# Kernel optimization log

Hardware: AMD Instinct MI355X
Metric: run time of the kernel (lower is better)

Reference implementation:

```python
import jax, jax.numpy as jnp
import numpy as np

WIN = (4, 8, 8)          # window_size (wd, wh, ww)
NUM_HEADS = 8
NW = 64                  # number of distinct shift-mask windows


def _relative_position_index(win):
    wd, wh, ww = win
    coords = np.stack(np.meshgrid(np.arange(wd), np.arange(wh), np.arange(ww), indexing='ij'))
    flat = coords.reshape(3, -1)                       # (3, N)
    rel = flat[:, :, None] - flat[:, None, :]          # (3, N, N)
    rel = rel.transpose(1, 2, 0).astype(np.int64)      # (N, N, 3)
    rel[..., 0] += wd - 1
    rel[..., 1] += wh - 1
    rel[..., 2] += ww - 1
    rel[..., 0] *= (2 * wh - 1) * (2 * ww - 1)
    rel[..., 1] *= (2 * ww - 1)
    return rel.sum(-1)                                 # (N, N)


def setup_inputs() -> dict:
    key = jax.random.key(0)
    ks = jax.random.split(key, 8)
    B_, C = 192, 256
    N = WIN[0] * WIN[1] * WIN[2]                       # 256 tokens per window
    table = (2 * WIN[0] - 1) * (2 * WIN[1] - 1) * (2 * WIN[2] - 1)  # 1575
    s = 0.02
    return {
        'x': jax.random.normal(ks[0], (B_, N, C), jnp.float32),
        'mask': jax.random.normal(ks[1], (NW, N, N), jnp.float32),
        'qkv_w': jax.random.normal(ks[2], (3 * C, C), jnp.float32) * s,
        'qkv_b': jax.random.normal(ks[3], (3 * C,), jnp.float32) * s,
        'proj_w': jax.random.normal(ks[4], (C, C), jnp.float32) * s,
        'proj_b': jax.random.normal(ks[5], (C,), jnp.float32) * s,
        'rel_pos_table': jax.random.normal(ks[6], (table, NUM_HEADS), jnp.float32) * s,
        'rel_pos_index': jnp.asarray(_relative_position_index(WIN), jnp.int32),
    }


def reference(x, mask, qkv_w, qkv_b, proj_w, proj_b, rel_pos_table, rel_pos_index):
    B_, N, C = x.shape
    H = NUM_HEADS
    hd = C // H
    scale = hd ** -0.5
    # qkv projection -> (3, B_, H, N, hd)
    qkv = (x @ qkv_w.T + qkv_b).reshape(B_, N, 3, H, hd).transpose(2, 0, 3, 1, 4)
    q, k, v = qkv[0], qkv[1], qkv[2]
    attn = jnp.einsum('bhnd,bhmd->bhnm', q * scale, k)            # (B_, H, N, N)
    # gathered relative-position bias: (N, N, H) -> (H, N, N)
    bias = rel_pos_table[rel_pos_index.reshape(-1)].reshape(N, N, H).transpose(2, 0, 1)
    attn = attn + bias[None]
    nW = mask.shape[0]
    attn = attn.reshape(B_ // nW, nW, H, N, N) + mask[None, :, None]
    attn = jax.nn.softmax(attn.reshape(B_, H, N, N), axis=-1)
    out = jnp.einsum('bhnm,bhmd->bhnd', attn, v)                  # (B_, H, N, hd)
    out = out.transpose(0, 2, 1, 3).reshape(B_, N, C)
    return out @ proj_w.T + proj_b
```

## Files before the change

kernel.cpp:

```cpp
#include <hip/hip_runtime.h>

typedef unsigned short ushort_t;
typedef __bf16 bf16x8 __attribute__((ext_vector_type(8)));
typedef float floatx4 __attribute__((ext_vector_type(4)));
typedef float floatx16 __attribute__((ext_vector_type(16)));

#define B_WIN 192
#define NTOK 256
#define CDIM 256
#define NHEAD 8
#define HDIM 32
#define NWIN 64
#define MROWS (B_WIN * NTOK)
#define LOG2E 1.4426950408889634f

__device__ __forceinline__ float uasf(unsigned int u) {
  float f; __builtin_memcpy(&f, &u, 4); return f;
}
__device__ __forceinline__ ushort_t f2bf(float f) {
  unsigned int u; __builtin_memcpy(&u, &f, 4);
  u = (u + 0x7fffu + ((u >> 16) & 1u)) >> 16;
  return (ushort_t)u;
}
__device__ __forceinline__ bf16x8 ldg8(const ushort_t* p) {
  return *reinterpret_cast<const bf16x8*>(p);
}
__device__ __forceinline__ void async_copy16(const void* g, void* l) {
  __builtin_amdgcn_global_load_lds(
      (const __attribute__((address_space(1))) unsigned int*)g,
      (__attribute__((address_space(3))) unsigned int*)l, 16, 0, 0);
}
__device__ __forceinline__ float fexp2(float x) {
  return __builtin_amdgcn_exp2f(x);
}
__device__ __forceinline__ unsigned pkbf(float a, float b) {
  return (unsigned)f2bf(a) | ((unsigned)f2bf(b) << 16);
}
__device__ __forceinline__ void plswap(unsigned& a, unsigned& b) {
  auto r = __builtin_amdgcn_permlane32_swap(a, b, false, false);
  a = r[0]; b = r[1];
}

__global__ __launch_bounds__(256) void cvt_f32_bf16(const float* __restrict__ src,
                                                    ushort_t* __restrict__ dst, int n8) {
  int t = blockIdx.x * 256 + threadIdx.x;
  if (t >= n8) return;
  const float4* s = reinterpret_cast<const float4*>(src) + (size_t)t * 2;
  float4 v0 = s[0], v1 = s[1];
  union { ushort_t u[8]; uint4 v; } pk;
  pk.u[0] = f2bf(v0.x); pk.u[1] = f2bf(v0.y); pk.u[2] = f2bf(v0.z); pk.u[3] = f2bf(v0.w);
  pk.u[4] = f2bf(v1.x); pk.u[5] = f2bf(v1.y); pk.u[6] = f2bf(v1.z); pk.u[7] = f2bf(v1.w);
  reinterpret_cast<uint4*>(dst)[t] = pk.v;
}

__global__ __launch_bounds__(256) void cvt_tile_w(const float* __restrict__ src,
                                                  ushort_t* __restrict__ dst, int n) {
  int t = blockIdx.x * 256 + threadIdx.x;
  if (t >= n) return;
  int col = t >> 5;
  int kk = (t & 31) * 8;
  const float4* s = reinterpret_cast<const float4*>(src + (size_t)col * 256 + kk);
  float4 v0 = s[0], v1 = s[1];
  union { ushort_t u[8]; uint4 v; } pk;
  pk.u[0] = f2bf(v0.x); pk.u[1] = f2bf(v0.y); pk.u[2] = f2bf(v0.z); pk.u[3] = f2bf(v0.w);
  pk.u[4] = f2bf(v1.x); pk.u[5] = f2bf(v1.y); pk.u[6] = f2bf(v1.z); pk.u[7] = f2bf(v1.w);
  size_t base = (size_t)(((col >> 4) * 8 + (kk >> 5)) * 512 + ((kk >> 3) & 3) * 128 + (col & 15) * 8);
  *reinterpret_cast<uint4*>(dst + base) = pk.v;
}

__global__ __launch_bounds__(256) void mask_prep(const float* __restrict__ mask,
                                                 ushort_t* __restrict__ mf) {
  const int win = blockIdx.x;
  const int qt = blockIdx.y;
  const int kb = blockIdx.z;
  const int l = threadIdx.x & 63;
  const int rg = threadIdx.x >> 6;
  const int tq = qt * 32 + (l & 31);
  const int hl = l >> 5;
  const int tk0 = kb * 32 + rg * 8 + hl * 4;
  const float4 mv = *reinterpret_cast<const float4*>(mask + (size_t)win * 65536 + tq * 256 + tk0);
  union { ushort_t u[4]; uint2 w; } pk;
  pk.u[0] = f2bf(mv.x * LOG2E); pk.u[1] = f2bf(mv.y * LOG2E);
  pk.u[2] = f2bf(mv.z * LOG2E); pk.u[3] = f2bf(mv.w * LOG2E);
  size_t base = ((size_t)((qt * 8 + kb) * 2 + (rg >> 1))) * 512 + l * 8 + (rg & 1) * 4;
  *reinterpret_cast<uint2*>(mf + ((size_t)win << 16) + base) = pk.w;
}

__global__ __launch_bounds__(256) void bias_prep(const int* __restrict__ idx,
                                                 const float* __restrict__ table,
                                                 ushort_t* __restrict__ bf) {
  const int qt = blockIdx.x;
  const int kb = blockIdx.y;
  const int l = threadIdx.x & 63;
  const int rg = threadIdx.x >> 6;
  const int tq = qt * 32 + (l & 31);
  const int hl = l >> 5;
  const int tk0 = kb * 32 + rg * 8 + hl * 4;
  const int4 ids = *reinterpret_cast<const int4*>(idx + tq * 256 + tk0);
  const int idarr[4] = {ids.x, ids.y, ids.z, ids.w};
  float v[8][4];
  #pragma unroll
  for (int r2 = 0; r2 < 4; ++r2) {
    const float* tr = table + (size_t)idarr[r2] * 8;
    float4 t0 = *reinterpret_cast<const float4*>(tr);
    float4 t1 = *reinterpret_cast<const float4*>(tr + 4);
    v[0][r2] = t0.x * LOG2E; v[1][r2] = t0.y * LOG2E;
    v[2][r2] = t0.z * LOG2E; v[3][r2] = t0.w * LOG2E;
    v[4][r2] = t1.x * LOG2E; v[5][r2] = t1.y * LOG2E;
    v[6][r2] = t1.z * LOG2E; v[7][r2] = t1.w * LOG2E;
  }
  size_t base = ((size_t)((qt * 8 + kb) * 2 + (rg >> 1))) * 512 + l * 8 + (rg & 1) * 4;
  #pragma unroll
  for (int h = 0; h < 8; ++h) {
    union { ushort_t u[4]; uint2 w; } pk;
    pk.u[0] = f2bf(v[h][0]); pk.u[1] = f2bf(v[h][1]);
    pk.u[2] = f2bf(v[h][2]); pk.u[3] = f2bf(v[h][3]);
    *reinterpret_cast<uint2*>(bf + ((size_t)h << 16) + base) = pk.w;
  }
}

__global__ __launch_bounds__(256) void qkv_gemm(
    const ushort_t* __restrict__ x, const ushort_t* __restrict__ wt,
    const float* __restrict__ qkvb, ushort_t* __restrict__ qws,
    ushort_t* __restrict__ kws, ushort_t* __restrict__ vtws) {
  const int lane = threadIdx.x & 63;
  const int wv = threadIdx.x >> 6;
  const int ln = lane & 15, qd = lane >> 4;
  const int b = blockIdx.x;
  const int xcd = b & 7, lb = b >> 3;
  const int rtile = xcd * 48 + (lb % 48);
  const int ctile = lb / 48;
  const int row0 = rtile * 128 + (wv >> 1) * 64;
  const int col0 = ctile * 128;
  const int colw = col0 + (wv & 1) * 64;

  floatx4 acc[4][4];
  #pragma unroll
  for (int rt = 0; rt < 4; ++rt)
    #pragma unroll
    for (int ct = 0; ct < 4; ++ct)
      acc[rt][ct] = floatx4{0.f, 0.f, 0.f, 0.f};

  const ushort_t* ap = x + (size_t)(row0 + ln) * 256 + qd * 8;
  const ushort_t* bp = wt + (size_t)col0 * 256 + (wv & 1) * 16384 + qd * 128 + ln * 8;
  bf16x8 abuf[2][4], bbuf[2][4];
  #pragma unroll
  for (int t = 0; t < 4; ++t) {
    abuf[0][t] = ldg8(ap + t * 16 * 256);
    abuf[1][t] = ldg8(ap + t * 16 * 256 + 32);
    bbuf[0][t] = ldg8(bp + (t * 8 + 0) * 512);
    bbuf[1][t] = ldg8(bp + (t * 8 + 1) * 512);
  }

  #pragma unroll
  for (int kt = 0; kt < 8; ++kt) {
    #pragma unroll
    for (int rt = 0; rt < 4; ++rt)
      #pragma unroll
      for (int ct = 0; ct < 4; ++ct)
        acc[rt][ct] = __builtin_amdgcn_mfma_f32_16x16x32_bf16(abuf[kt & 1][rt], bbuf[kt & 1][ct],
                                                              acc[rt][ct], 0, 0, 0);
    if (kt < 6) {
      #pragma unroll
      for (int t = 0; t < 4; ++t) {
        abuf[kt & 1][t] = ldg8(ap + t * 16 * 256 + (kt + 2) * 32);
        bbuf[kt & 1][t] = ldg8(bp + (t * 8 + kt + 2) * 512);
      }
    }
  }

  const int s = colw >> 8;
  const float SCLQ = 0.17677669529663687f * LOG2E;
  #pragma unroll
  for (int ct = 0; ct < 4; ++ct) {
    int colg = colw + ct * 16 + ln;
    float bcol = qkvb[colg];
    int cs = colg & 255;
    int h = cs >> 5, d = cs & 31;
    int dslice = d >> 4, hh = (d >> 3) & 1, j = d & 7;
    #pragma unroll
    for (int rt = 0; rt < 4; ++rt) {
      int rbase = row0 + rt * 16 + qd * 4;
      int bwin = rbase >> 8, tok0 = rbase & 255;
      size_t slab = (size_t)(bwin * 8 + h) * 8192;
      if (s == 2) {
        int kt2 = tok0 >> 4, h2 = (tok0 >> 3) & 1, jj = tok0 & 7;
        union { ushort_t u[4]; uint2 v; } pk;
        #pragma unroll
        for (int i = 0; i < 4; ++i) pk.u[i] = f2bf(acc[rt][ct][i] + bcol);
        *reinterpret_cast<uint2*>(vtws + slab + kt2 * 512 + h2 * 256 + d * 8 + jj) = pk.v;
      } else {
        int blk = tok0 >> 5, c0 = tok0 & 31;
        size_t base = slab + (size_t)((blk * 2 + dslice) * 512 + hh * 256 + c0 * 8 + j);
        if (s == 0) {
          #pragma unroll
          for (int i = 0; i < 4; ++i)
            qws[base + i * 8] = f2bf((acc[rt][ct][i] + bcol) * SCLQ);
        } else {
          #pragma unroll
          for (int i = 0; i < 4; ++i)
            kws[base + i * 8] = f2bf(acc[rt][ct][i] + bcol);
        }
      }
    }
  }
}

__global__ __launch_bounds__(512, 4) void attn_kernel(
    const ushort_t* __restrict__ qws, const ushort_t* __restrict__ kws,
    const ushort_t* __restrict__ vtws, const ushort_t* __restrict__ mf,
    const ushort_t* __restrict__ bfr, ushort_t* __restrict__ aows) {
  __shared__ __align__(16) ushort_t lds_kv[16384];
  __shared__ float inv_lds[256];
  const int lane = threadIdx.x & 63;
  const int wv = threadIdx.x >> 6;
  const int t = blockIdx.x;
  const int batch = t % 3;
  const int wh = t / 3;
  const int win = wh >> 3, h = wh & 7;
  const int bwin = batch * 64 + win;
  const int bh = bwin * 8 + h;

  {
    const char* kg = (const char*)(kws + (size_t)bh * 8192);
    const char* vg = (const char*)(vtws + (size_t)bh * 8192);
    #pragma unroll
    for (int r = 0; r < 2; ++r) {
      int off = r * 8192 + wv * 1024;
      async_copy16(kg + off + lane * 16, (char*)lds_kv + off);
      async_copy16(vg + off + lane * 16, (char*)lds_kv + 16384 + off);
    }
  }
  __syncthreads();

  const int qt = wv;
  const int hl = lane >> 5;
  const ushort_t* qb = qws + (size_t)bh * 8192 + qt * 1024 + lane * 8;
  const bf16x8 qf0 = ldg8(qb);
  const bf16x8 qf1 = ldg8(qb + 512);
  const ushort_t* mp = mf + ((size_t)win << 16) + qt * 8192 + lane * 8;
  const ushort_t* cp = bfr + ((size_t)h << 16) + qt * 8192 + lane * 8;

  floatx16 o;
  #pragma unroll
  for (int i = 0; i < 16; ++i) o[i] = 0.f;
  float ss0 = 0.f, ss1 = 0.f, ss2 = 0.f, ss3 = 0.f;

  #pragma unroll
  for (int kb = 0; kb < 8; ++kb) {
    const uint4 m0 = *reinterpret_cast<const uint4*>(mp + kb * 1024);
    const uint4 m1 = *reinterpret_cast<const uint4*>(mp + kb * 1024 + 512);
    const uint4 c0 = *reinterpret_cast<const uint4*>(cp + kb * 1024);
    const uint4 c1 = *reinterpret_cast<const uint4*>(cp + kb * 1024 + 512);
    floatx16 st;
    st[0]  = uasf(m0.x << 16) + uasf(c0.x << 16);
    st[1]  = uasf(m0.x & 0xffff0000u) + uasf(c0.x & 0xffff0000u);
    st[2]  = uasf(m0.y << 16) + uasf(c0.y << 16);
    st[3]  = uasf(m0.y & 0xffff0000u) + uasf(c0.y & 0xffff0000u);
    st[4]  = uasf(m0.z << 16) + uasf(c0.z << 16);
    st[5]  = uasf(m0.z & 0xffff0000u) + uasf(c0.z & 0xffff0000u);
    st[6]  = uasf(m0.w << 16) + uasf(c0.w << 16);
    st[7]  = uasf(m0.w & 0xffff0000u) + uasf(c0.w & 0xffff0000u);
    st[8]  = uasf(m1.x << 16) + uasf(c1.x << 16);
    st[9]  = uasf(m1.x & 0xffff0000u) + uasf(c1.x & 0xffff0000u);
    st[10] = uasf(m1.y << 16) + uasf(c1.y << 16);
    st[11] = uasf(m1.y & 0xffff0000u) + uasf(c1.y & 0xffff0000u);
    st[12] = uasf(m1.z << 16) + uasf(c1.z << 16);
    st[13] = uasf(m1.z & 0xffff0000u) + uasf(c1.z & 0xffff0000u);
    st[14] = uasf(m1.w << 16) + uasf(c1.w << 16);
    st[15] = uasf(m1.w & 0xffff0000u) + uasf(c1.w & 0xffff0000u);

    const bf16x8 kf0 = *reinterpret_cast<const bf16x8*>(&lds_kv[(kb * 2 + 0) * 512 + lane * 8]);
    const bf16x8 kf1 = *reinterpret_cast<const bf16x8*>(&lds_kv[(kb * 2 + 1) * 512 + lane * 8]);
    st = __builtin_amdgcn_mfma_f32_32x32x16_bf16(kf0, qf0, st, 0, 0, 0);
    st = __builtin_amdgcn_mfma_f32_32x32x16_bf16(kf1, qf1, st, 0, 0, 0);

    #pragma unroll
    for (int i = 0; i < 16; i += 4) {
      float e0 = fexp2(st[i]);     st[i]     = e0; ss0 += e0;
      float e1 = fexp2(st[i + 1]); st[i + 1] = e1; ss1 += e1;
      float e2 = fexp2(st[i + 2]); st[i + 2] = e2; ss2 += e2;
      float e3 = fexp2(st[i + 3]); st[i + 3] = e3; ss3 += e3;
    }

    unsigned p0 = pkbf(st[0], st[1]),   p1 = pkbf(st[2], st[3]);
    unsigned p2 = pkbf(st[4], st[5]),   p3 = pkbf(st[6], st[7]);
    unsigned p4 = pkbf(st[8], st[9]),   p5 = pkbf(st[10], st[11]);
    unsigned p6 = pkbf(st[12], st[13]), p7 = pkbf(st[14], st[15]);
    plswap(p0, p2);
    plswap(p1, p3);
    plswap(p4, p6);
    plswap(p5, p7);
    union { unsigned u[4]; bf16x8 v; } afe, afo;
    afe.u[0] = p0; afe.u[1] = p1; afe.u[2] = p2; afe.u[3] = p3;
    afo.u[0] = p4; afo.u[1] = p5; afo.u[2] = p6; afo.u[3] = p7;

    const bf16x8 bv0 = *reinterpret_cast<const bf16x8*>(&lds_kv[8192 + (kb * 2 + 0) * 512 + lane * 8]);
    const bf16x8 bv1 = *reinterpret_cast<const bf16x8*>(&lds_kv[8192 + (kb * 2 + 1) * 512 + lane * 8]);
    o = __builtin_amdgcn_mfma_f32_32x32x16_bf16(afe.v, bv0, o, 0, 0, 0);
    o = __builtin_amdgcn_mfma_f32_32x32x16_bf16(afo.v, bv1, o, 0, 0, 0);
  }

  float ssum = (ss0 + ss1) + (ss2 + ss3);
  ssum += __shfl_xor(ssum, 32, 64);
  const float inv = 1.0f / ssum;
  inv_lds[wv * 32 + (lane & 31)] = inv;
  __builtin_amdgcn_s_waitcnt(0);
  const float4 iv0 = *reinterpret_cast<const float4*>(&inv_lds[wv * 32 + 0 + hl * 4]);
  const float4 iv1 = *reinterpret_cast<const float4*>(&inv_lds[wv * 32 + 8 + hl * 4]);
  const float4 iv2 = *reinterpret_cast<const float4*>(&inv_lds[wv * 32 + 16 + hl * 4]);
  const float4 iv3 = *reinterpret_cast<const float4*>(&inv_lds[wv * 32 + 24 + hl * 4]);

  const int d = lane & 31;
  ushort_t* op = aows + (((size_t)bwin * 256 + qt * 32 + 4 * hl) << 8) + h * 32 + d;
  op[0 * 256]  = f2bf(o[0]  * iv0.x); op[1 * 256]  = f2bf(o[1]  * iv0.y);
  op[2 * 256]  = f2bf(o[2]  * iv0.z); op[3 * 256]  = f2bf(o[3]  * iv0.w);
  op[8 * 256]  = f2bf(o[4]  * iv1.x); op[9 * 256]  = f2bf(o[5]  * iv1.y);
  op[10 * 256] = f2bf(o[6]  * iv1.z); op[11 * 256] = f2bf(o[7]  * iv1.w);
  op[16 * 256] = f2bf(o[8]  * iv2.x); op[17 * 256] = f2bf(o[9]  * iv2.y);
  op[18 * 256] = f2bf(o[10] * iv2.z); op[19 * 256] = f2bf(o[11] * iv2.w);
  op[24 * 256] = f2bf(o[12] * iv3.x); op[25 * 256] = f2bf(o[13] * iv3.y);
  op[26 * 256] = f2bf(o[14] * iv3.z); op[27 * 256] = f2bf(o[15] * iv3.w);
}

__global__ __launch_bounds__(256) void proj_gemm(
    const ushort_t* __restrict__ a_, const ushort_t* __restrict__ wt,
    const float* __restrict__ pb, float* __restrict__ out) {
  const int lane = threadIdx.x & 63;
  const int wv = threadIdx.x >> 6;
  const int ln = lane & 15, qd = lane >> 4;
  const int b = blockIdx.x;
  const int xcd = b & 7, lb = b >> 3;
  const int rtile = xcd * 48 + (lb % 48);
  const int ctile = lb / 48;
  const int row0 = rtile * 128 + (wv >> 1) * 64;
  const int col0 = ctile * 128;
  const int colw = col0 + (wv & 1) * 64;

  floatx4 acc[4][4];
  #pragma unroll
  for (int rt = 0; rt < 4; ++rt)
    #pragma unroll
    for (int ct = 0; ct < 4; ++ct)
      acc[rt][ct] = floatx4{0.f, 0.f, 0.f, 0.f};

  const ushort_t* ap = a_ + (size_t)(row0 + ln) * 256 + qd * 8;
  const ushort_t* bp = wt + (size_t)col0 * 256 + (wv & 1) * 16384 + qd * 128 + ln * 8;
  bf16x8 abuf[2][4], bbuf[2][4];
  #pragma unroll
  for (int t = 0; t < 4; ++t) {
    abuf[0][t] = ldg8(ap + t * 16 * 256);
    abuf[1][t] = ldg8(ap + t * 16 * 256 + 32);
    bbuf[0][t] = ldg8(bp + (t * 8 + 0) * 512);
    bbuf[1][t] = ldg8(bp + (t * 8 + 1) * 512);
  }

  #pragma unroll
  for (int kt = 0; kt < 8; ++kt) {
    #pragma unroll
    for (int rt = 0; rt < 4; ++rt)
      #pragma unroll
      for (int ct = 0; ct < 4; ++ct)
        acc[rt][ct] = __builtin_amdgcn_mfma_f32_16x16x32_bf16(abuf[kt & 1][rt], bbuf[kt & 1][ct],
                                                              acc[rt][ct], 0, 0, 0);
    if (kt < 6) {
      #pragma unroll
      for (int t = 0; t < 4; ++t) {
        abuf[kt & 1][t] = ldg8(ap + t * 16 * 256 + (kt + 2) * 32);
        bbuf[kt & 1][t] = ldg8(bp + (t * 8 + kt + 2) * 512);
      }
    }
  }

  #pragma unroll
  for (int ct = 0; ct < 4; ++ct) {
    int colg = colw + ct * 16 + ln;
    float bcol = pb[colg];
    #pragma unroll
    for (int rt = 0; rt < 4; ++rt) {
      int rbase = row0 + rt * 16 + qd * 4;
      #pragma unroll
      for (int i = 0; i < 4; ++i)
        out[(size_t)(rbase + i) * 256 + colg] = acc[rt][ct][i] + bcol;
    }
  }
}

extern "C" void kernel_launch(void* const* d_in, const int* in_sizes, int n_in,
                              void* d_out, int out_size, void* d_ws, size_t ws_size,
                              hipStream_t stream) {
  const float* x      = (const float*)d_in[0];
  const float* mask   = (const float*)d_in[1];
  const float* qkv_w  = (const float*)d_in[2];
  const float* qkv_b  = (const float*)d_in[3];
  const float* proj_w = (const float*)d_in[4];
  const float* proj_b = (const float*)d_in[5];
  const float* table  = (const float*)d_in[6];
  const int*   idx    = (const int*)d_in[7];
  float* out = (float*)d_out;

  char* ws = (char*)d_ws;
  const size_t SZ = (size_t)MROWS * CDIM * 2;
  ushort_t* xbf  = (ushort_t*)(ws);
  ushort_t* qws  = (ushort_t*)(ws + SZ);
  ushort_t* kws  = (ushort_t*)(ws + 2 * SZ);
  ushort_t* vtws = (ushort_t*)(ws + 3 * SZ);
  ushort_t* aows = (ushort_t*)(ws + 4 * SZ);
  ushort_t* mfws = (ushort_t*)(ws + 5 * SZ);
  ushort_t* bfws = (ushort_t*)(ws + 5 * SZ + 8388608);
  ushort_t* wqkvbf  = (ushort_t*)(ws + 5 * SZ + 8388608 + 1048576);
  ushort_t* wprojbf = (ushort_t*)(ws + 5 * SZ + 8388608 + 1048576 + 393216);

  cvt_f32_bf16<<<dim3(6144), dim3(256), 0, stream>>>(x, xbf, 12582912 / 8);
  cvt_tile_w<<<dim3(96), dim3(256), 0, stream>>>(qkv_w, wqkvbf, 768 * 32);
  cvt_tile_w<<<dim3(32), dim3(256), 0, stream>>>(proj_w, wprojbf, 256 * 32);
  mask_prep<<<dim3(64, 8, 8), dim3(256), 0, stream>>>(mask, mfws);
  bias_prep<<<dim3(8, 8), dim3(256), 0, stream>>>(idx, table, bfws);
  qkv_gemm<<<dim3(2304), dim3(256), 0, stream>>>(xbf, wqkvbf, qkv_b, qws, kws, vtws);
  attn_kernel<<<dim3(1536), dim3(512), 0, stream>>>(qws, kws, vtws, mfws, bfws, aows);
  proj_gemm<<<dim3(768), dim3(256), 0, stream>>>(aows, wprojbf, proj_b, out);
}
```

Baseline: 272.2 us.

## Stage GEMM operands through LDS with async copies and pre-tiled activation layouts

Both projection GEMMs now copy A and B tiles into double-buffered LDS using global_load_lds async copies, instead of each wave loading its fragments directly from global memory into registers. To make each 1 KB chunk contiguous, x is converted into the same MFMA-tiled bf16 layout already used for the weights, and the attention kernel writes its output in that tiled layout for proj_gemm. The goal is fully coalesced, DMA-style global loads with operand reuse across waves. In exchange it adds 32 KB of LDS per block and a barrier every k-step, which may reduce occupancy.

```diff
diff --git a/kernel.cpp b/kernel.cpp
--- a/kernel.cpp
+++ b/kernel.cpp
@@ -41,30 +41,18 @@
   a = r[0]; b = r[1];
 }
 
-__global__ __launch_bounds__(256) void cvt_f32_bf16(const float* __restrict__ src,
-                                                    ushort_t* __restrict__ dst, int n8) {
+__global__ __launch_bounds__(256) void cvt_tile_w(const float* __restrict__ src,
+                                                  ushort_t* __restrict__ dst, int n) {
   int t = blockIdx.x * 256 + threadIdx.x;
-  if (t >= n8) return;
-  const float4* s = reinterpret_cast<const float4*>(src) + (size_t)t * 2;
+  if (t >= n) return;
+  int row = t >> 5;
+  int kk = (t & 31) * 8;
+  const float4* s = reinterpret_cast<const float4*>(src + (size_t)row * 256 + kk);
   float4 v0 = s[0], v1 = s[1];
   union { ushort_t u[8]; uint4 v; } pk;
   pk.u[0] = f2bf(v0.x); pk.u[1] = f2bf(v0.y); pk.u[2] = f2bf(v0.z); pk.u[3] = f2bf(v0.w);
   pk.u[4] = f2bf(v1.x); pk.u[5] = f2bf(v1.y); pk.u[6] = f2bf(v1.z); pk.u[7] = f2bf(v1.w);
-  reinterpret_cast<uint4*>(dst)[t] = pk.v;
-}
-
-__global__ __launch_bounds__(256) void cvt_tile_w(const float* __restrict__ src,
-                                                  ushort_t* __restrict__ dst, int n) {
-  int t = blockIdx.x * 256 + threadIdx.x;
-  if (t >= n) return;
-  int col = t >> 5;
-  int kk = (t & 31) * 8;
-  const float4* s = reinterpret_cast<const float4*>(src + (size_t)col * 256 + kk);
-  float4 v0 = s[0], v1 = s[1];
-  union { ushort_t u[8]; uint4 v; } pk;
-  pk.u[0] = f2bf(v0.x); pk.u[1] = f2bf(v0.y); pk.u[2] = f2bf(v0.z); pk.u[3] = f2bf(v0.w);
-  pk.u[4] = f2bf(v1.x); pk.u[5] = f2bf(v1.y); pk.u[6] = f2bf(v1.z); pk.u[7] = f2bf(v1.w);
-  size_t base = (size_t)(((col >> 4) * 8 + (kk >> 5)) * 512 + ((kk >> 3) & 3) * 128 + (col & 15) * 8);
+  size_t base = (size_t)(((row >> 4) * 8 + (kk >> 5)) * 512 + ((kk >> 3) & 3) * 128 + (row & 15) * 8);
   *reinterpret_cast<uint4*>(dst + base) = pk.v;
 }
 
@@ -123,6 +111,7 @@
     const ushort_t* __restrict__ x, const ushort_t* __restrict__ wt,
     const float* __restrict__ qkvb, ushort_t* __restrict__ qws,
     ushort_t* __restrict__ kws, ushort_t* __restrict__ vtws) {
+  __shared__ __align__(16) char lds[32768];
   const int lane = threadIdx.x & 63;
   const int wv = threadIdx.x >> 6;
   const int ln = lane & 15, qd = lane >> 4;
@@ -131,8 +120,10 @@
   const int rtile = xcd * 48 + (lb % 48);
   const int ctile = lb / 48;
   const int row0 = rtile * 128 + (wv >> 1) * 64;
-  const int col0 = ctile * 128;
-  const int colw = col0 + (wv & 1) * 64;
+  const int colw = ctile * 128 + (wv & 1) * 64;
+
+  const char* ag = (const char*)x + (size_t)rtile * 65536;
+  const char* bg = (const char*)wt + (size_t)ctile * 65536;
 
   floatx4 acc[4][4];
   #pragma unroll
@@ -141,33 +132,43 @@
     for (int ct = 0; ct < 4; ++ct)
       acc[rt][ct] = floatx4{0.f, 0.f, 0.f, 0.f};
 
-  const ushort_t* ap = x + (size_t)(row0 + ln) * 256 + qd * 8;
-  const ushort_t* bp = wt + (size_t)col0 * 256 + (wv & 1) * 16384 + qd * 128 + ln * 8;
-  bf16x8 abuf[2][4], bbuf[2][4];
-  #pragma unroll
-  for (int t = 0; t < 4; ++t) {
-    abuf[0][t] = ldg8(ap + t * 16 * 256);
-    abuf[1][t] = ldg8(ap + t * 16 * 256 + 32);
-    bbuf[0][t] = ldg8(bp + (t * 8 + 0) * 512);
-    bbuf[1][t] = ldg8(bp + (t * 8 + 1) * 512);
-  }
-
+  #define STAGE(buf, kt)                                                          \
+    {                                                                             \
+      _Pragma("unroll")                                                           \
+      for (int c2 = 0; c2 < 2; ++c2) {                                            \
+        int c = wv * 2 + c2;                                                      \
+        async_copy16(ag + (((size_t)c * 8 + (kt)) << 10) + lane * 16,             \
+                     lds + (buf) * 8192 + c * 1024);                              \
+        async_copy16(bg + (((size_t)c * 8 + (kt)) << 10) + lane * 16,             \
+                     lds + 16384 + (buf) * 8192 + c * 1024);                      \
+      }                                                                           \
+    }
+
+  STAGE(0, 0);
+  __syncthreads();
+
+  int cur = 0;
   #pragma unroll
   for (int kt = 0; kt < 8; ++kt) {
+    if (kt < 7) STAGE(cur ^ 1, kt + 1);
+    const char* ab = lds + cur * 8192 + ((wv >> 1) * 4) * 1024 + qd * 256 + ln * 16;
+    const char* bb = lds + 16384 + cur * 8192 + ((wv & 1) * 4) * 1024 + qd * 256 + ln * 16;
+    bf16x8 a[4], bq[4];
+    #pragma unroll
+    for (int t = 0; t < 4; ++t) {
+      a[t] = *reinterpret_cast<const bf16x8*>(ab + t * 1024);
+      bq[t] = *reinterpret_cast<const bf16x8*>(bb + t * 1024);
+    }
     #pragma unroll
     for (int rt = 0; rt < 4; ++rt)
       #pragma unroll
       for (int ct = 0; ct < 4; ++ct)
-        acc[rt][ct] = __builtin_amdgcn_mfma_f32_16x16x32_bf16(abuf[kt & 1][rt], bbuf[kt & 1][ct],
+        acc[rt][ct] = __builtin_amdgcn_mfma_f32_16x16x32_bf16(a[rt], bq[ct],
                                                               acc[rt][ct], 0, 0, 0);
-    if (kt < 6) {
-      #pragma unroll
-      for (int t = 0; t < 4; ++t) {
-        abuf[kt & 1][t] = ldg8(ap + t * 16 * 256 + (kt + 2) * 32);
-        bbuf[kt & 1][t] = ldg8(bp + (t * 8 + kt + 2) * 512);
-      }
-    }
-  }
+    if (kt < 7) __syncthreads();
+    cur ^= 1;
+  }
+  #undef STAGE
 
   const int s = colw >> 8;
   const float SCLQ = 0.17677669529663687f * LOG2E;
@@ -312,20 +313,30 @@
   const float4 iv3 = *reinterpret_cast<const float4*>(&inv_lds[wv * 32 + 24 + hl * 4]);
 
   const int d = lane & 31;
-  ushort_t* op = aows + (((size_t)bwin * 256 + qt * 32 + 4 * hl) << 8) + h * 32 + d;
-  op[0 * 256]  = f2bf(o[0]  * iv0.x); op[1 * 256]  = f2bf(o[1]  * iv0.y);
-  op[2 * 256]  = f2bf(o[2]  * iv0.z); op[3 * 256]  = f2bf(o[3]  * iv0.w);
-  op[8 * 256]  = f2bf(o[4]  * iv1.x); op[9 * 256]  = f2bf(o[5]  * iv1.y);
-  op[10 * 256] = f2bf(o[6]  * iv1.z); op[11 * 256] = f2bf(o[7]  * iv1.w);
-  op[16 * 256] = f2bf(o[8]  * iv2.x); op[17 * 256] = f2bf(o[9]  * iv2.y);
-  op[18 * 256] = f2bf(o[10] * iv2.z); op[19 * 256] = f2bf(o[11] * iv2.w);
-  op[24 * 256] = f2bf(o[12] * iv3.x); op[25 * 256] = f2bf(o[13] * iv3.y);
-  op[26 * 256] = f2bf(o[14] * iv3.z); op[27 * 256] = f2bf(o[15] * iv3.w);
+  ushort_t* op = aows + (((size_t)(bwin * 16 + 2 * qt) * 8 + h) << 9)
+                 + ((d >> 3) & 3) * 128 + hl * 32 + (d & 7);
+  op[0 * 8]              = f2bf(o[0]  * iv0.x);
+  op[1 * 8]              = f2bf(o[1]  * iv0.y);
+  op[2 * 8]              = f2bf(o[2]  * iv0.z);
+  op[3 * 8]              = f2bf(o[3]  * iv0.w);
+  op[64 + 0 * 8]         = f2bf(o[4]  * iv1.x);
+  op[64 + 1 * 8]         = f2bf(o[5]  * iv1.y);
+  op[64 + 2 * 8]         = f2bf(o[6]  * iv1.z);
+  op[64 + 3 * 8]         = f2bf(o[7]  * iv1.w);
+  op[4096 + 0 * 8]       = f2bf(o[8]  * iv2.x);
+  op[4096 + 1 * 8]       = f2bf(o[9]  * iv2.y);
+  op[4096 + 2 * 8]       = f2bf(o[10] * iv2.z);
+  op[4096 + 3 * 8]       = f2bf(o[11] * iv2.w);
+  op[4096 + 64 + 0 * 8]  = f2bf(o[12] * iv3.x);
+  op[4096 + 64 + 1 * 8]  = f2bf(o[13] * iv3.y);
+  op[4096 + 64 + 2 * 8]  = f2bf(o[14] * iv3.z);
+  op[4096 + 64 + 3 * 8]  = f2bf(o[15] * iv3.w);
 }
 
 __global__ __launch_bounds__(256) void proj_gemm(
     const ushort_t* __restrict__ a_, const ushort_t* __restrict__ wt,
     const float* __restrict__ pb, float* __restrict__ out) {
+  __shared__ __align__(16) char lds[32768];
   const int lane = threadIdx.x & 63;
   const int wv = threadIdx.x >> 6;
   const int ln = lane & 15, qd = lane >> 4;
@@ -334,8 +345,10 @@
   const int rtile = xcd * 48 + (lb % 48);
   const int ctile = lb / 48;
   const int row0 = rtile * 128 + (wv >> 1) * 64;
-  const int col0 = ctile * 128;
-  const int colw = col0 + (wv & 1) * 64;
+  const int colw = ctile * 128 + (wv & 1) * 64;
+
+  const char* ag = (const char*)a_ + (size_t)rtile * 65536;
+  const char* bg = (const char*)wt + (size_t)ctile * 65536;
 
   floatx4 acc[4][4];
   #pragma unroll
@@ -344,33 +357,43 @@
     for (int ct = 0; ct < 4; ++ct)
       acc[rt][ct] = floatx4{0.f, 0.f, 0.f, 0.f};
 
-  const ushort_t* ap = a_ + (size_t)(row0 + ln) * 256 + qd * 8;
-  const ushort_t* bp = wt + (size_t)col0 * 256 + (wv & 1) * 16384 + qd * 128 + ln * 8;
-  bf16x8 abuf[2][4], bbuf[2][4];
-  #pragma unroll
-  for (int t = 0; t < 4; ++t) {
-    abuf[0][t] = ldg8(ap + t * 16 * 256);
-    abuf[1][t] = ldg8(ap + t * 16 * 256 + 32);
-    bbuf[0][t] = ldg8(bp + (t * 8 + 0) * 512);
-    bbuf[1][t] = ldg8(bp + (t * 8 + 1) * 512);
-  }
-
+  #define STAGE(buf, kt)                                                          \
+    {                                                                             \
+      _Pragma("unroll")                                                           \
+      for (int c2 = 0; c2 < 2; ++c2) {                                            \
+        int c = wv * 2 + c2;                                                      \
+        async_copy16(ag + (((size_t)c * 8 + (kt)) << 10) + lane * 16,             \
+                     lds + (buf) * 8192 + c * 1024);                              \
+        async_copy16(bg + (((size_t)c * 8 + (kt)) << 10) + lane * 16,             \
+                     lds + 16384 + (buf) * 8192 + c * 1024);                      \
+      }                                                                           \
+    }
+
+  STAGE(0, 0);
+  __syncthreads();
+
+  int cur = 0;
   #pragma unroll
   for (int kt = 0; kt < 8; ++kt) {
+    if (kt < 7) STAGE(cur ^ 1, kt + 1);
+    const char* ab = lds + cur * 8192 + ((wv >> 1) * 4) * 1024 + qd * 256 + ln * 16;
+    const char* bb = lds + 16384 + cur * 8192 + ((wv & 1) * 4) * 1024 + qd * 256 + ln * 16;
+    bf16x8 a[4], bq[4];
+    #pragma unroll
+    for (int t = 0; t < 4; ++t) {
+      a[t] = *reinterpret_cast<const bf16x8*>(ab + t * 1024);
+      bq[t] = *reinterpret_cast<const bf16x8*>(bb + t * 1024);
+    }
     #pragma unroll
     for (int rt = 0; rt < 4; ++rt)
       #pragma unroll
       for (int ct = 0; ct < 4; ++ct)
-        acc[rt][ct] = __builtin_amdgcn_mfma_f32_16x16x32_bf16(abuf[kt & 1][rt], bbuf[kt & 1][ct],
+        acc[rt][ct] = __builtin_amdgcn_mfma_f32_16x16x32_bf16(a[rt], bq[ct],
                                                               acc[rt][ct], 0, 0, 0);
-    if (kt < 6) {
-      #pragma unroll
-      for (int t = 0; t < 4; ++t) {
-        abuf[kt & 1][t] = ldg8(ap + t * 16 * 256 + (kt + 2) * 32);
-        bbuf[kt & 1][t] = ldg8(bp + (t * 8 + kt + 2) * 512);
-      }
-    }
-  }
+    if (kt < 7) __syncthreads();
+    cur ^= 1;
+  }
+  #undef STAGE
 
   #pragma unroll
   for (int ct = 0; ct < 4; ++ct) {
@@ -411,7 +434,7 @@
   ushort_t* wqkvbf  = (ushort_t*)(ws + 5 * SZ + 8388608 + 1048576);
   ushort_t* wprojbf = (ushort_t*)(ws + 5 * SZ + 8388608 + 1048576 + 393216);
 
-  cvt_f32_bf16<<<dim3(6144), dim3(256), 0, stream>>>(x, xbf, 12582912 / 8);
+  cvt_tile_w<<<dim3(6144), dim3(256), 0, stream>>>(x, xbf, MROWS * 32);
   cvt_tile_w<<<dim3(96), dim3(256), 0, stream>>>(qkv_w, wqkvbf, 768 * 32);
   cvt_tile_w<<<dim3(32), dim3(256), 0, stream>>>(proj_w, wprojbf, 256 * 32);
   mask_prep<<<dim3(64, 8, 8), dim3(256), 0, stream>>>(mask, mfws);
```

Result: faster. 250.0 us (-8.2%).
